# Kernel optimization log

Hardware: AMD Instinct MI355X
Metric: run time of the kernel (lower is better)

## Reference

```python
import jax, jax.numpy as jnp
import numpy as np

NODE_DIM = 128
CTX_DIM = 256
OUT_DIM = 256
GRID_SIZE = 4
SPLINE_ORDER = 3
IN_DIM = 3 * NODE_DIM  # subj + obj + transformed context
N_NODES = 100000
N_EDGES = 100000


def make_grid(in_dim, grid_size, spline_order, grid_range=(-1.0, 1.0)):
    h = (grid_range[1] - grid_range[0]) / grid_size
    g = (np.arange(-spline_order, grid_size + spline_order + 1, dtype=np.float32) * h
         + grid_range[0])  # [grid_size + 2*spline_order + 1]
    return jnp.asarray(np.tile(g[None, :], (in_dim, 1)))  # [in, G]


def b_splines(x, grid, spline_order):
    # x: [N, in], grid: [in, G] -> bases: [N, in, grid_size + spline_order]
    xg = x[:, :, None]
    bases = ((xg >= grid[:, :-1]) & (xg < grid[:, 1:])).astype(x.dtype)
    for k in range(1, spline_order + 1):
        left = (xg - grid[:, : -(k + 1)]) / (grid[:, k:-1] - grid[:, : -(k + 1)]) * bases[..., :-1]
        right = (grid[:, k + 1:] - xg) / (grid[:, k + 1:] - grid[:, 1:-k]) * bases[..., 1:]
        bases = left + right
    return bases


def setup_inputs() -> dict:
    key = jax.random.key(0)
    ks = jax.random.split(key, 8)
    n_coef = GRID_SIZE + SPLINE_ORDER
    return {
        "node_embeddings": jax.random.normal(ks[0], (N_NODES, NODE_DIM), jnp.float32),
        "context_embeddings": jax.random.normal(ks[1], (N_EDGES, CTX_DIM), jnp.float32),
        "pair_indices": jax.random.randint(ks[2], (N_EDGES, 2), 0, N_NODES, jnp.int64 if jax.config.jax_enable_x64 else jnp.int32),
        "ctx_w": jax.random.normal(ks[3], (NODE_DIM, CTX_DIM), jnp.float32) * (1.0 / np.sqrt(CTX_DIM)),
        "ctx_b": jnp.zeros((NODE_DIM,), jnp.float32),
        "base_weight": jax.random.normal(ks[4], (OUT_DIM, IN_DIM), jnp.float32) * (1.0 / np.sqrt(IN_DIM)),
        "spline_weight": jax.random.normal(ks[5], (OUT_DIM, IN_DIM, n_coef), jnp.float32) * 0.1,
        "spline_scaler": jax.random.normal(ks[6], (OUT_DIM, IN_DIM), jnp.float32) * (1.0 / np.sqrt(IN_DIM)),
        "grid": make_grid(IN_DIM, GRID_SIZE, SPLINE_ORDER),
    }


def reference(node_embeddings, context_embeddings, pair_indices, ctx_w, ctx_b,
              base_weight, spline_weight, spline_scaler, grid):
    # gather subject/object node embeddings (irregular access)
    subj = node_embeddings[pair_indices[:, 0]]          # [E, node_dim]
    obj = node_embeddings[pair_indices[:, 1]]           # [E, node_dim]
    ctx = context_embeddings @ ctx_w.T + ctx_b          # [E, node_dim]
    x = jnp.concatenate([subj, obj, ctx], axis=1)       # [E, 3*node_dim]

    # efficient-KAN linear layer: base (SiLU) branch + B-spline branch
    base_out = jax.nn.silu(x) @ base_weight.T           # [E, out]
    bsp = b_splines(x, grid, SPLINE_ORDER)              # [E, in, n_coef]
    scaled_w = spline_weight * spline_scaler[:, :, None]  # [out, in, n_coef]
    spline_out = jnp.einsum('nic,oic->no', bsp, scaled_w)
    return base_out + spline_out
```

## Files before the change

### kernel.cpp

```cpp
#include <hip/hip_runtime.h>

#define NEDGES   100000
#define NODE_DIM 128
#define CTX_DIM  256
#define OUT_DIM  256
#define IN_DIM   384
#define NCOEF    7

#define BM2      128
#define BK2      32
#define NCH2     96
#define THR2     512

typedef __bf16 bf16x8 __attribute__((ext_vector_type(8)));
typedef float  f32x4  __attribute__((ext_vector_type(4)));

static __device__ __forceinline__ unsigned short f2bf(float f) {
    unsigned int u = __float_as_uint(f);
    u += 0x7FFFu + ((u >> 16) & 1u);
    return (unsigned short)(u >> 16);
}
static __device__ __forceinline__ float bf2f(unsigned short h) {
    return __uint_as_float(((unsigned int)h) << 16);
}
static __device__ __forceinline__ unsigned int pkbf(float a, float b) {
    unsigned int ua = __float_as_uint(a), ub = __float_as_uint(b);
    ua += 0x7FFFu + ((ua >> 16) & 1u);
    ub += 0x7FFFu + ((ub >> 16) & 1u);
    return (ua >> 16) | (ub & 0xFFFF0000u);
}
static __device__ __forceinline__ float silu(float x) {
    return x / (1.0f + __expf(-x));
}
static __device__ __forceinline__ float n3(float t) {
    float d2 = t - 2.0f;
    float a  = fabsf(d2);
    float p1 = fmaf(fmaf(0.5f, a, -1.0f), d2 * d2, 0.66666667f);
    float dd = fmaxf(2.0f - a, 0.0f);
    float p2 = dd * dd * (dd * (1.0f / 6.0f));
    return a < 1.0f ? p1 : p2;
}

static __device__ __forceinline__ void glds16(const unsigned short* g, unsigned short* l) {
    __builtin_amdgcn_global_load_lds(
        (const __attribute__((address_space(1))) void*)g,
        (__attribute__((address_space(3))) void*)l, 16, 0, 0);
}

__global__ void prep_w2(const float* __restrict__ base_w,
                        const float* __restrict__ spline_w,
                        const float* __restrict__ spline_s,
                        unsigned short* __restrict__ Wsw)
{
    int o = blockIdx.x;
    int i = threadIdx.x;
    int bi = o * IN_DIM + i;
    float sc = spline_s[bi];
    const float* sw = spline_w + (size_t)bi * NCOEF;
    uint4 v;
    v.x = pkbf(base_w[bi], sw[0] * sc);
    v.y = pkbf(sw[1] * sc, sw[2] * sc);
    v.z = pkbf(sw[3] * sc, sw[4] * sc);
    v.w = pkbf(sw[5] * sc, sw[6] * sc);
    int ch = i >> 2, g8 = i & 3;
    int p  = o * 4 + (((o >> 1) + g8) & 3);
    *(uint4*)(Wsw + (size_t)ch * (OUT_DIM * BK2) + p * 8) = v;
}

__global__ void prep_ctxw(const float* __restrict__ ctx_w,
                          unsigned short* __restrict__ B)
{
    int n  = blockIdx.x;
    int k4 = threadIdx.x;
    float4 v = *(const float4*)(ctx_w + (size_t)n * CTX_DIM + k4 * 4);
    *(uint2*)&B[(size_t)n * CTX_DIM + k4 * 4] =
        make_uint2(pkbf(v.x, v.y), pkbf(v.z, v.w));
}

#define A2STR  40
#define A2SZ   (BM2 * A2STR)
#define B2SZ   (OUT_DIM * BK2)
#define OFF_A0 0
#define OFF_A1 A2SZ
#define OFF_B0 (2 * A2SZ)
#define OFF_B1 (2 * A2SZ + B2SZ)
#define LDS2   (2 * A2SZ + 2 * B2SZ)
#define CG_STR 72
#define CG_ESTR 136

static __device__ __forceinline__ void gen_elem(
    float x, float hinv, float b0, unsigned short* dst)
{
    float sl = silu(x);
    unsigned short slh = f2bf(sl);
    float t  = fmaf(x, hinv, b0);
    float jf = floorf(t);
    int   j0 = (int)jf;
    float u  = t - jf;
    float u2 = u * u, u3 = u2 * u;
    float Q0 = u3 * 0.16666667f;
    float d  = 1.0f - u;
    float Q3 = d * d * d * 0.16666667f;
    float Q1 = fmaf(0.5f, u + u2 - u3, 0.16666667f);
    float Q2 = fmaf(0.5f, u3, 0.66666667f - u2);
    unsigned plo = pkbf(Q3, Q2);
    unsigned phi = pkbf(Q1, Q0);
    unsigned long long P = ((unsigned long long)phi << 32) | plo;
    int sh = (j0 << 4) - 32;
    unsigned a  = (unsigned)sh;
    unsigned na = 0u - a;
    unsigned long long lo =
        (a  < 64u) ? (P << (a  & 63u)) : ((na < 64u) ? (P >> (na & 63u)) : 0ull);
    unsigned b2 = a - 64u;
    unsigned nb = 0u - b2;
    unsigned long long hi =
        (b2 < 64u) ? (P << (b2 & 63u)) : ((nb < 64u) ? (P >> (nb & 63u)) : 0ull);
    lo = (lo & ~0xFFFFull) | (unsigned long long)slh;
    uint4 w;
    w.x = (unsigned)lo; w.y = (unsigned)(lo >> 32);
    w.z = (unsigned)hi; w.w = (unsigned)(hi >> 32);
    *(uint4*)dst = w;
}

static __device__ __forceinline__ float fetchx(
    const float* ps, const float* po, const unsigned short* pc, int ch)
{
    if (ch < 32) return ps[ch << 2];
    if (ch < 64) return po[(ch - 32) << 2];
    return bf2f(pc[(ch - 64) << 2]);
}

__global__ __launch_bounds__(THR2, 4)
void kan_gemm2(const unsigned short* __restrict__ Wsw,
               const float* __restrict__ ctx_emb,
               const unsigned short* __restrict__ ctxwB,
               const float* __restrict__ ctx_b,
               unsigned short* __restrict__ CtxB,
               const float* __restrict__ node_emb,
               const int*   __restrict__ pair,
               const float* __restrict__ grid,
               float* __restrict__ out)
{
    __shared__ unsigned short smem[LDS2];
    const int tid    = threadIdx.x;
    const int e_base = blockIdx.x * BM2;
    const int wid    = tid >> 6;
    const int lan    = tid & 63;
    const int lrow   = lan & 15;
    const int lquad  = lan >> 4;
    const int m0     = (wid & 1) * 64;
    const int n0     = (wid >> 1) * 64;

    {
        f32x4 cacc[4][2];
        #pragma unroll
        for (int a = 0; a < 4; ++a)
            #pragma unroll
            for (int b = 0; b < 2; ++b) { f32x4 z = {0.f,0.f,0.f,0.f}; cacc[a][b] = z; }
        const int cn0 = (wid >> 1) * 32;

        #pragma unroll
        for (int it = 0; it < 4; ++it) {
            int id = it * THR2 + tid;
            int r  = id >> 4;
            int c4 = id & 15;
            int eg = e_base + r; if (eg >= NEDGES) eg = NEDGES - 1;
            float4 v = *(const float4*)(ctx_emb + (size_t)eg * CTX_DIM + c4 * 4);
            *(uint2*)&smem[r * CG_STR + c4 * 4] = make_uint2(pkbf(v.x, v.y), pkbf(v.z, v.w));
        }
        __syncthreads();

        for (int kc = 0; kc < 4; ++kc) {
            if (kc + 1 < 4) {
                unsigned short* nb = smem + ((kc + 1) & 1) * (128 * CG_STR);
                #pragma unroll
                for (int it = 0; it < 4; ++it) {
                    int id = it * THR2 + tid;
                    int r  = id >> 4;
                    int c4 = id & 15;
                    int eg = e_base + r; if (eg >= NEDGES) eg = NEDGES - 1;
                    float4 v = *(const float4*)(ctx_emb + (size_t)eg * CTX_DIM + (kc + 1) * 64 + c4 * 4);
                    *(uint2*)&nb[r * CG_STR + c4 * 4] = make_uint2(pkbf(v.x, v.y), pkbf(v.z, v.w));
                }
            }
            const unsigned short* sa = smem + (kc & 1) * (128 * CG_STR);
            #pragma unroll
            for (int ks = 0; ks < 2; ++ks) {
                int koff = ks * 32 + lquad * 8;
                bf16x8 caf[4], cbf[2];
                #pragma unroll
                for (int mt = 0; mt < 4; ++mt)
                    caf[mt] = *(const bf16x8*)&sa[(m0 + mt*16 + lrow) * CG_STR + koff];
                #pragma unroll
                for (int nt = 0; nt < 2; ++nt)
                    cbf[nt] = *(const bf16x8*)&ctxwB[(size_t)(cn0 + nt*16 + lrow) * CTX_DIM + kc * 64 + koff];
                #pragma unroll
                for (int mt = 0; mt < 4; ++mt)
                    #pragma unroll
                    for (int nt = 0; nt < 2; ++nt)
                        cacc[mt][nt] = __builtin_amdgcn_mfma_f32_16x16x32_bf16(
                            caf[mt], cbf[nt], cacc[mt][nt], 0, 0, 0);
            }
            __syncthreads();
        }

        #pragma unroll
        for (int nt = 0; nt < 2; ++nt) {
            int col = cn0 + nt * 16 + lrow;
            float cb = ctx_b[col];
            #pragma unroll
            for (int mt = 0; mt < 4; ++mt)
                #pragma unroll
                for (int r = 0; r < 4; ++r) {
                    int row = m0 + mt * 16 + lquad * 4 + r;
                    smem[row * CG_ESTR + col] = f2bf(cacc[mt][nt][r] + cb);
                }
        }
        __syncthreads();
        #pragma unroll
        for (int it = 0; it < 8; ++it) {
            int id  = it * THR2 + tid;
            int row = id >> 5;
            int g   = id & 31;
            int eg  = e_base + row; if (eg >= NEDGES) eg = NEDGES - 1;
            *(uint2*)&CtxB[(size_t)eg * 128 + g * 4] = *(uint2*)&smem[row * CG_ESTR + g * 4];
        }
        __syncthreads();
    }

    const float g0   = grid[0];
    const float hinv = 1.0f / (grid[1] - grid[0]);
    const float b0   = -g0 * hinv;

    const int grow = tid >> 2;
    const int gcol = tid & 3;
    int geg = e_base + grow; if (geg >= NEDGES) geg = NEDGES - 1;
    const int nsub = pair[geg * 2 + 0];
    const int nobj = pair[geg * 2 + 1];
    const float* ps = node_emb + (size_t)nsub * NODE_DIM + gcol;
    const float* po = node_emb + (size_t)nobj * NODE_DIM + gcol;
    const unsigned short* pc = CtxB + (size_t)geg * 128 + gcol;
    const unsigned awr = grow * A2STR + gcol * 8;

    f32x4 acc[4][4];
    #pragma unroll
    for (int a = 0; a < 4; ++a)
        #pragma unroll
        for (int b = 0; b < 4; ++b) { f32x4 z = {0.f,0.f,0.f,0.f}; acc[a][b] = z; }

    float xc = fetchx(ps, po, pc, 0);
    float xn = fetchx(ps, po, pc, 1);

    #pragma unroll
    for (int it = 0; it < 2; ++it) {
        int id = it * THR2 + tid;
        glds16(Wsw + id * 8, &smem[OFF_B0 + id * 8]);
    }
    gen_elem(xc, hinv, b0, &smem[OFF_A0 + awr]);
    __syncthreads();

    for (int kb = 0; kb < NCH2; ++kb) {
        const int cur = kb & 1;
        if (kb + 1 < NCH2) {
            float xh = xn;
            if (kb + 2 < NCH2) xn = fetchx(ps, po, pc, kb + 2);
            const unsigned short* wc = Wsw + (size_t)(kb + 1) * B2SZ;
            unsigned boff = cur ? OFF_B0 : OFF_B1;
            #pragma unroll
            for (int it = 0; it < 2; ++it) {
                int id = it * THR2 + tid;
                glds16(wc + id * 8, &smem[boff + id * 8]);
            }
            gen_elem(xh, hinv, b0, &smem[(cur ? OFF_A0 : OFF_A1) + awr]);
        }
        const unsigned ab = cur ? OFF_A1 : OFF_A0;
        const unsigned bb = cur ? OFF_B1 : OFF_B0;
        bf16x8 af[4], bfr[4];
        #pragma unroll
        for (int mt = 0; mt < 4; ++mt)
            af[mt] = *(const bf16x8*)&smem[ab + (m0 + mt*16 + lrow) * A2STR + lquad * 8];
        #pragma unroll
        for (int nt = 0; nt < 4; ++nt) {
            int n = n0 + nt * 16 + lrow;
            bfr[nt] = *(const bf16x8*)&smem[bb + n * 32 + ((((n >> 1) + lquad) & 3) << 3)];
        }
        #pragma unroll
        for (int mt = 0; mt < 4; ++mt)
            #pragma unroll
            for (int nt = 0; nt < 4; ++nt)
                acc[mt][nt] = __builtin_amdgcn_mfma_f32_16x16x32_bf16(
                    af[mt], bfr[nt], acc[mt][nt], 0, 0, 0);
        __syncthreads();
    }

    #pragma unroll
    for (int mt = 0; mt < 4; ++mt) {
        #pragma unroll
        for (int r = 0; r < 4; ++r) {
            int row = m0 + mt * 16 + lquad * 4 + r;
            int eg  = e_base + row;
            if (eg < NEDGES) {
                float* op = out + (size_t)eg * OUT_DIM + n0 + lrow;
                #pragma unroll
                for (int nt = 0; nt < 4; ++nt)
                    op[nt * 16] = acc[mt][nt][r];
            }
        }
    }
}

#define XSTR 392
#define FSTR 72
#define FOFF_X 0
#define FOFF_A (128 * XSTR)
#define FOFF_B (FOFF_A + 128 * FSTR)
#define FLDS (FOFF_B + OUT_DIM * FSTR)

__global__ __launch_bounds__(512, 2)
void fused_fallback(const float* __restrict__ node_emb,
                    const float* __restrict__ ctx_emb,
                    const int*   __restrict__ pair,
                    const float* __restrict__ ctx_w,
                    const float* __restrict__ ctx_b,
                    const float* __restrict__ base_w,
                    const float* __restrict__ spline_w,
                    const float* __restrict__ spline_s,
                    const float* __restrict__ grid,
                    float* __restrict__ out)
{
    __shared__ unsigned short smem[FLDS];
    const int tid    = threadIdx.x;
    const int e_base = blockIdx.x * 128;
    const int wid    = tid >> 6;
    const int lan    = tid & 63;
    const int lrow   = lan & 15;
    const int lquad  = lan >> 4;

    #pragma unroll
    for (int it = 0; it < 16; ++it) {
        int id    = it * 512 + tid;
        int lane4 = id & 31;
        int e     = (id >> 5) & 127;
        int which = id >> 12;
        int eg = e_base + e; if (eg >= NEDGES) eg = NEDGES - 1;
        int node = pair[eg * 2 + which];
        const float4 v = *(const float4*)(node_emb + (size_t)node * NODE_DIM + lane4 * 4);
        *(ushort4*)&smem[FOFF_X + e * XSTR + which * NODE_DIM + lane4 * 4] =
            make_ushort4(f2bf(v.x), f2bf(v.y), f2bf(v.z), f2bf(v.w));
    }
    {
        f32x4 cacc[4][2];
        #pragma unroll
        for (int a = 0; a < 4; ++a)
            #pragma unroll
            for (int b = 0; b < 2; ++b) { f32x4 z = {0.f,0.f,0.f,0.f}; cacc[a][b] = z; }
        const int m0 = (wid & 1) * 64;
        const int n0 = (wid >> 1) * 32;
        for (int kc = 0; kc < 4; ++kc) {
            #pragma unroll
            for (int it = 0; it < 4; ++it) {
                int id = it * 512 + tid;
                int r  = id >> 4;
                int c4 = id & 15;
                int eg = e_base + r; if (eg >= NEDGES) eg = NEDGES - 1;
                float4 v = *(const float4*)(ctx_emb + (size_t)eg * CTX_DIM + kc * 64 + c4 * 4);
                *(ushort4*)&smem[FOFF_A + r * FSTR + c4 * 4] =
                    make_ushort4(f2bf(v.x), f2bf(v.y), f2bf(v.z), f2bf(v.w));
                float4 w = *(const float4*)(ctx_w + (size_t)r * CTX_DIM + kc * 64 + c4 * 4);
                *(ushort4*)&smem[FOFF_B + r * FSTR + c4 * 4] =
                    make_ushort4(f2bf(w.x), f2bf(w.y), f2bf(w.z), f2bf(w.w));
            }
            __syncthreads();
            #pragma unroll
            for (int ks = 0; ks < 2; ++ks) {
                int koff = ks * 32 + lquad * 8;
                bf16x8 af[4], bfr[2];
                #pragma unroll
                for (int mt = 0; mt < 4; ++mt)
                    af[mt] = *(const bf16x8*)&smem[FOFF_A + (m0 + mt*16 + lrow) * FSTR + koff];
                #pragma unroll
                for (int nt = 0; nt < 2; ++nt)
                    bfr[nt] = *(const bf16x8*)&smem[FOFF_B + (n0 + nt*16 + lrow) * FSTR + koff];
                #pragma unroll
                for (int mt = 0; mt < 4; ++mt)
                    #pragma unroll
                    for (int nt = 0; nt < 2; ++nt)
                        cacc[mt][nt] = __builtin_amdgcn_mfma_f32_16x16x32_bf16(
                            af[mt], bfr[nt], cacc[mt][nt], 0, 0, 0);
            }
            __syncthreads();
        }
        #pragma unroll
        for (int mt = 0; mt < 4; ++mt)
            #pragma unroll
            for (int nt = 0; nt < 2; ++nt)
                #pragma unroll
                for (int r = 0; r < 4; ++r) {
                    int row = m0 + mt*16 + lquad*4 + r;
                    int col = n0 + nt*16 + lrow;
                    smem[FOFF_X + row * XSTR + 256 + col] = f2bf(cacc[mt][nt][r] + ctx_b[col]);
                }
    }
    __syncthreads();

    const float g0   = grid[0];
    const float hinv = 1.0f / (grid[1] - grid[0]);

    f32x4 acc[4][4];
    #pragma unroll
    for (int a = 0; a < 4; ++a)
        #pragma unroll
        for (int b = 0; b < 4; ++b) { f32x4 z = {0.f,0.f,0.f,0.f}; acc[a][b] = z; }

    const int m0 = (wid & 1) * 64;
    const int n0 = (wid >> 1) * 64;

    for (int kb = 0; kb < 48; ++kb) {
        const int seg = kb / 6;
        const int i0  = (kb - seg * 6) * 64;
        #pragma unroll
        for (int it = 0; it < 4; ++it) {
            int id = it * 512 + tid;
            int e  = id >> 4;
            int qq = id & 15;
            ushort4 xv = *(const ushort4*)&smem[FOFF_X + e * XSTR + i0 + qq * 4];
            float x0 = bf2f(xv.x), x1 = bf2f(xv.y), x2 = bf2f(xv.z), x3 = bf2f(xv.w);
            unsigned short r0, r1, r2, r3;
            if (seg == 0) {
                r0 = f2bf(silu(x0)); r1 = f2bf(silu(x1));
                r2 = f2bf(silu(x2)); r3 = f2bf(silu(x3));
            } else {
                const float cf = (float)(seg - 1);
                r0 = f2bf(n3((x0 - g0) * hinv - cf));
                r1 = f2bf(n3((x1 - g0) * hinv - cf));
                r2 = f2bf(n3((x2 - g0) * hinv - cf));
                r3 = f2bf(n3((x3 - g0) * hinv - cf));
            }
            *(ushort4*)&smem[FOFF_A + e * FSTR + qq * 4] = make_ushort4(r0, r1, r2, r3);
        }
        #pragma unroll
        for (int it = 0; it < 4; ++it) {
            int id = it * 512 + tid;
            int o  = id >> 4;
            int qq = id & 15;
            unsigned short r0, r1, r2, r3;
            if (seg == 0) {
                const float4 w = *(const float4*)(base_w + (size_t)o * IN_DIM + i0 + qq * 4);
                r0 = f2bf(w.x); r1 = f2bf(w.y); r2 = f2bf(w.z); r3 = f2bf(w.w);
            } else {
                int c  = seg - 1;
                int bi = o * IN_DIM + i0 + qq * 4;
                r0 = f2bf(spline_w[(size_t)(bi    ) * NCOEF + c] * spline_s[bi    ]);
                r1 = f2bf(spline_w[(size_t)(bi + 1) * NCOEF + c] * spline_s[bi + 1]);
                r2 = f2bf(spline_w[(size_t)(bi + 2) * NCOEF + c] * spline_s[bi + 2]);
                r3 = f2bf(spline_w[(size_t)(bi + 3) * NCOEF + c] * spline_s[bi + 3]);
            }
            *(ushort4*)&smem[FOFF_B + o * FSTR + qq * 4] = make_ushort4(r0, r1, r2, r3);
        }
        __syncthreads();
        #pragma unroll
        for (int ks = 0; ks < 2; ++ks) {
            int koff = ks * 32 + lquad * 8;
            bf16x8 af[4], bfr[4];
            #pragma unroll
            for (int mt = 0; mt < 4; ++mt)
                af[mt] = *(const bf16x8*)&smem[FOFF_A + (m0 + mt*16 + lrow) * FSTR + koff];
            #pragma unroll
            for (int nt = 0; nt < 4; ++nt)
                bfr[nt] = *(const bf16x8*)&smem[FOFF_B + (n0 + nt*16 + lrow) * FSTR + koff];
            #pragma unroll
            for (int mt = 0; mt < 4; ++mt)
                #pragma unroll
                for (int nt = 0; nt < 4; ++nt)
                    acc[mt][nt] = __builtin_amdgcn_mfma_f32_16x16x32_bf16(
                        af[mt], bfr[nt], acc[mt][nt], 0, 0, 0);
        }
        __syncthreads();
    }

    #pragma unroll
    for (int mt = 0; mt < 4; ++mt) {
        #pragma unroll
        for (int r = 0; r < 4; ++r) {
            int row = m0 + mt*16 + lquad*4 + r;
            int eg  = e_base + row;
            if (eg < NEDGES) {
                float* op = out + (size_t)eg * OUT_DIM + n0 + lrow;
                #pragma unroll
                for (int nt = 0; nt < 4; ++nt)
                    op[nt * 16] = acc[mt][nt][r];
            }
        }
    }
}

extern "C" void kernel_launch(void* const* d_in, const int* in_sizes, int n_in,
                              void* d_out, int out_size, void* d_ws, size_t ws_size,
                              hipStream_t stream)
{
    const float* node_emb = (const float*)d_in[0];
    const float* ctx_emb  = (const float*)d_in[1];
    const int*   pair     = (const int*)d_in[2];
    const float* ctx_w    = (const float*)d_in[3];
    const float* ctx_b    = (const float*)d_in[4];
    const float* base_w   = (const float*)d_in[5];
    const float* spline_w = (const float*)d_in[6];
    const float* spline_s = (const float*)d_in[7];
    const float* grid     = (const float*)d_in[8];
    float* out = (float*)d_out;

    const int nblk = (NEDGES + BM2 - 1) / BM2;
    const size_t ctxwoff = 1572864u;
    const size_t xoff    = 2u * 1024u * 1024u;
    const size_t need = xoff + (size_t)NEDGES * 128 * sizeof(unsigned short);

    if (ws_size >= need) {
        unsigned short* Wsw   = (unsigned short*)d_ws;
        unsigned short* CtxwB = (unsigned short*)((char*)d_ws + ctxwoff);
        unsigned short* CtxB  = (unsigned short*)((char*)d_ws + xoff);
        prep_w2<<<OUT_DIM, IN_DIM, 0, stream>>>(base_w, spline_w, spline_s, Wsw);
        prep_ctxw<<<128, 64, 0, stream>>>(ctx_w, CtxwB);
        kan_gemm2<<<nblk, THR2, 0, stream>>>(
            Wsw, ctx_emb, CtxwB, ctx_b, CtxB, node_emb, pair, grid, out);
    } else {
        fused_fallback<<<nblk, 512, 0, stream>>>(
            node_emb, ctx_emb, pair, ctx_w, ctx_b, base_w, spline_w, spline_s, grid, out);
    }
}
```

Measured before the change: 435.4 us.

## Triple-buffer weight tiles with two-stage prefetch and partial vmcnt waits

Switches the B (weight) LDS staging from double to triple buffering, issuing global-to-LDS loads two k-blocks ahead. The full __syncthreads is replaced by s_waitcnt with a nonzero vmcnt plus s_barrier, so the newest in-flight weight loads and the x fetch need not finish before the next iteration. The aim is to hide global latency for the weight stream. In exchange it uses more LDS, which may lower occupancy, and correctness depends on hand-counted vmcnt values matching the instructions the compiler emits.

```diff
diff --git a/kernel.cpp b/kernel.cpp
--- a/kernel.cpp
+++ b/kernel.cpp
@@ -83,8 +83,7 @@
 #define OFF_A0 0
 #define OFF_A1 A2SZ
 #define OFF_B0 (2 * A2SZ)
-#define OFF_B1 (2 * A2SZ + B2SZ)
-#define LDS2   (2 * A2SZ + 2 * B2SZ)
+#define LDS2   (2 * A2SZ + 3 * B2SZ)
 #define CG_STR 72
 #define CG_ESTR 136
 
@@ -251,30 +250,39 @@
     float xc = fetchx(ps, po, pc, 0);
     float xn = fetchx(ps, po, pc, 1);
 
+    unsigned bcur = OFF_B0, bnxt = OFF_B0 + B2SZ, bnx2 = OFF_B0 + 2 * B2SZ;
+
     #pragma unroll
     for (int it = 0; it < 2; ++it) {
         int id = it * THR2 + tid;
-        glds16(Wsw + id * 8, &smem[OFF_B0 + id * 8]);
+        glds16(Wsw + id * 8, &smem[bcur + id * 8]);
+    }
+    #pragma unroll
+    for (int it = 0; it < 2; ++it) {
+        int id = it * THR2 + tid;
+        glds16(Wsw + B2SZ + id * 8, &smem[bnxt + id * 8]);
     }
     gen_elem(xc, hinv, b0, &smem[OFF_A0 + awr]);
-    __syncthreads();
+    asm volatile("s_waitcnt lgkmcnt(0)\n\ts_waitcnt vmcnt(2)" ::: "memory");
+    __builtin_amdgcn_s_barrier();
+    asm volatile("" ::: "memory");
 
     for (int kb = 0; kb < NCH2; ++kb) {
         const int cur = kb & 1;
-        if (kb + 1 < NCH2) {
-            float xh = xn;
-            if (kb + 2 < NCH2) xn = fetchx(ps, po, pc, kb + 2);
-            const unsigned short* wc = Wsw + (size_t)(kb + 1) * B2SZ;
-            unsigned boff = cur ? OFF_B0 : OFF_B1;
+        float xh = xn;
+        if (kb + 2 < NCH2) {
+            xn = fetchx(ps, po, pc, kb + 2);
+            const unsigned short* wc = Wsw + (size_t)(kb + 2) * B2SZ;
             #pragma unroll
             for (int it = 0; it < 2; ++it) {
                 int id = it * THR2 + tid;
-                glds16(wc + id * 8, &smem[boff + id * 8]);
-            }
+                glds16(wc + id * 8, &smem[bnx2 + id * 8]);
+            }
+        }
+        if (kb + 1 < NCH2)
             gen_elem(xh, hinv, b0, &smem[(cur ? OFF_A0 : OFF_A1) + awr]);
-        }
+
         const unsigned ab = cur ? OFF_A1 : OFF_A0;
-        const unsigned bb = cur ? OFF_B1 : OFF_B0;
         bf16x8 af[4], bfr[4];
         #pragma unroll
         for (int mt = 0; mt < 4; ++mt)
@@ -282,7 +290,7 @@
         #pragma unroll
         for (int nt = 0; nt < 4; ++nt) {
             int n = n0 + nt * 16 + lrow;
-            bfr[nt] = *(const bf16x8*)&smem[bb + n * 32 + ((((n >> 1) + lquad) & 3) << 3)];
+            bfr[nt] = *(const bf16x8*)&smem[bcur + n * 32 + ((((n >> 1) + lquad) & 3) << 3)];
         }
         #pragma unroll
         for (int mt = 0; mt < 4; ++mt)
@@ -290,7 +298,16 @@
             for (int nt = 0; nt < 4; ++nt)
                 acc[mt][nt] = __builtin_amdgcn_mfma_f32_16x16x32_bf16(
                     af[mt], bfr[nt], acc[mt][nt], 0, 0, 0);
-        __syncthreads();
+
+        if (kb + 1 < NCH2) {
+            if (kb + 2 < NCH2)
+                asm volatile("s_waitcnt lgkmcnt(0)\n\ts_waitcnt vmcnt(3)" ::: "memory");
+            else
+                asm volatile("s_waitcnt lgkmcnt(0)\n\ts_waitcnt vmcnt(0)" ::: "memory");
+            __builtin_amdgcn_s_barrier();
+            asm volatile("" ::: "memory");
+        }
+        unsigned tmp = bcur; bcur = bnxt; bnxt = bnx2; bnx2 = tmp;
     }
 
     #pragma unroll
```

New measurement: 433.6 us. Within noise of the previous version (-0.4%).

## Load weight fragments directly from global into registers instead of LDS staging

Applied to the files above, without the earlier changes.

The prepacked weight matrix is reordered so that each lane can read its MFMA B fragment straight from global memory, which removes the LDS double buffer for weights and the LDS reads that fed them. The next chunk's fragments are loaded into registers right after the MFMAs, and the full __syncthreads is replaced by an LDS-only waitcnt plus s_barrier so that global loads can stay in flight across the barrier. This shrinks LDS usage and LDS traffic, but every wave now re-reads the weights from L2/global, which raises cache traffic and exposes load latency. The launch bound is also lowered to 2 blocks per SM.

```diff
diff --git a/kernel.cpp b/kernel.cpp
--- a/kernel.cpp
+++ b/kernel.cpp
@@ -39,12 +39,6 @@
     float dd = fmaxf(2.0f - a, 0.0f);
     float p2 = dd * dd * (dd * (1.0f / 6.0f));
     return a < 1.0f ? p1 : p2;
-}
-
-static __device__ __forceinline__ void glds16(const unsigned short* g, unsigned short* l) {
-    __builtin_amdgcn_global_load_lds(
-        (const __attribute__((address_space(1))) void*)g,
-        (__attribute__((address_space(3))) void*)l, 16, 0, 0);
 }
 
 __global__ void prep_w2(const float* __restrict__ base_w,
@@ -62,9 +56,8 @@
     v.y = pkbf(sw[1] * sc, sw[2] * sc);
     v.z = pkbf(sw[3] * sc, sw[4] * sc);
     v.w = pkbf(sw[5] * sc, sw[6] * sc);
-    int ch = i >> 2, g8 = i & 3;
-    int p  = o * 4 + (((o >> 1) + g8) & 3);
-    *(uint4*)(Wsw + (size_t)ch * (OUT_DIM * BK2) + p * 8) = v;
+    int ch = i >> 2, ii = i & 3;
+    *(uint4*)(Wsw + (size_t)((ch * 4 + ii) * 256 + o) * 8) = v;
 }
 
 __global__ void prep_ctxw(const float* __restrict__ ctx_w,
@@ -79,14 +72,11 @@
 
 #define A2STR  40
 #define A2SZ   (BM2 * A2STR)
-#define B2SZ   (OUT_DIM * BK2)
 #define OFF_A0 0
 #define OFF_A1 A2SZ
-#define OFF_B0 (2 * A2SZ)
-#define OFF_B1 (2 * A2SZ + B2SZ)
-#define LDS2   (2 * A2SZ + 2 * B2SZ)
 #define CG_STR 72
 #define CG_ESTR 136
+#define LDS2   (2 * 128 * CG_STR)
 
 static __device__ __forceinline__ void gen_elem(
     float x, float hinv, float b0, unsigned short* dst)
@@ -130,7 +120,7 @@
     return bf2f(pc[(ch - 64) << 2]);
 }
 
-__global__ __launch_bounds__(THR2, 4)
+__global__ __launch_bounds__(THR2, 2)
 void kan_gemm2(const unsigned short* __restrict__ Wsw,
                const float* __restrict__ ctx_emb,
                const unsigned short* __restrict__ ctxwB,
@@ -242,6 +232,8 @@
     const unsigned short* pc = CtxB + (size_t)geg * 128 + gcol;
     const unsigned awr = grow * A2STR + gcol * 8;
 
+    const unsigned short* wbase = Wsw + ((size_t)lquad * 256 + n0 + lrow) * 8;
+
     f32x4 acc[4][4];
     #pragma unroll
     for (int a = 0; a < 4; ++a)
@@ -251,46 +243,45 @@
     float xc = fetchx(ps, po, pc, 0);
     float xn = fetchx(ps, po, pc, 1);
 
+    bf16x8 bfr[4];
     #pragma unroll
-    for (int it = 0; it < 2; ++it) {
-        int id = it * THR2 + tid;
-        glds16(Wsw + id * 8, &smem[OFF_B0 + id * 8]);
-    }
+    for (int nt = 0; nt < 4; ++nt)
+        bfr[nt] = *(const bf16x8*)(wbase + nt * 128);
     gen_elem(xc, hinv, b0, &smem[OFF_A0 + awr]);
-    __syncthreads();
+    asm volatile("s_waitcnt lgkmcnt(0)" ::: "memory");
+    __builtin_amdgcn_s_barrier();
+    asm volatile("" ::: "memory");
 
     for (int kb = 0; kb < NCH2; ++kb) {
         const int cur = kb & 1;
-        if (kb + 1 < NCH2) {
-            float xh = xn;
-            if (kb + 2 < NCH2) xn = fetchx(ps, po, pc, kb + 2);
-            const unsigned short* wc = Wsw + (size_t)(kb + 1) * B2SZ;
-            unsigned boff = cur ? OFF_B0 : OFF_B1;
-            #pragma unroll
-            for (int it = 0; it < 2; ++it) {
-                int id = it * THR2 + tid;
-                glds16(wc + id * 8, &smem[boff + id * 8]);
-            }
+        float xh = xn;
+        if (kb + 2 < NCH2) xn = fetchx(ps, po, pc, kb + 2);
+        if (kb + 1 < NCH2)
             gen_elem(xh, hinv, b0, &smem[(cur ? OFF_A0 : OFF_A1) + awr]);
-        }
+
         const unsigned ab = cur ? OFF_A1 : OFF_A0;
-        const unsigned bb = cur ? OFF_B1 : OFF_B0;
-        bf16x8 af[4], bfr[4];
+        bf16x8 af[4];
         #pragma unroll
         for (int mt = 0; mt < 4; ++mt)
             af[mt] = *(const bf16x8*)&smem[ab + (m0 + mt*16 + lrow) * A2STR + lquad * 8];
-        #pragma unroll
-        for (int nt = 0; nt < 4; ++nt) {
-            int n = n0 + nt * 16 + lrow;
-            bfr[nt] = *(const bf16x8*)&smem[bb + n * 32 + ((((n >> 1) + lquad) & 3) << 3)];
-        }
+
         #pragma unroll
         for (int mt = 0; mt < 4; ++mt)
             #pragma unroll
             for (int nt = 0; nt < 4; ++nt)
                 acc[mt][nt] = __builtin_amdgcn_mfma_f32_16x16x32_bf16(
                     af[mt], bfr[nt], acc[mt][nt], 0, 0, 0);
-        __syncthreads();
+
+        if (kb + 1 < NCH2) {
+            const unsigned short* wnx = wbase + (size_t)(kb + 1) * 8192;
+            #pragma unroll
+            for (int nt = 0; nt < 4; ++nt)
+                bfr[nt] = *(const bf16x8*)(wnx + nt * 128);
+
+            asm volatile("s_waitcnt lgkmcnt(0)" ::: "memory");
+            __builtin_amdgcn_s_barrier();
+            asm volatile("" ::: "memory");
+        }
     }
 
     #pragma unroll
@@ -523,7 +514,8 @@
         kan_gemm2<<<nblk, THR2, 0, stream>>>(
             Wsw, ctx_emb, CtxwB, ctx_b, CtxB, node_emb, pair, grid, out);
     } else {
-        fused_fallback<<<nblk, 512, 0, stream>>>(
+        const int nblkf = (NEDGES + 127) / 128;
+        fused_fallback<<<nblkf, 512, 0, stream>>>(
             node_emb, ctx_emb, pair, ctx_w, ctx_b, base_w, spline_w, spline_s, grid, out);
     }
 }
```

After: 544.5 us. 1.25x slower.
